# Optimization experiments

Hardware: AMD Instinct MI355X
Metric: run time of the kernel (lower is better)

## Reference

```python
import jax, jax.numpy as jnp
import numpy as np

N_NODES = 50000
N_EDGES = 800000
N_GRAPHS = 256
F_IN = 75  # num_features_xd


def _lin_params(key, fan_in, fan_out):
    kw, kb = jax.random.split(key)
    s = 1.0 / np.sqrt(fan_in)
    W = jax.random.uniform(kw, (fan_in, fan_out), jnp.float32, -s, s)
    b = jax.random.uniform(kb, (fan_out,), jnp.float32, -s, s)
    return W, b


def setup_inputs() -> dict:
    key = jax.random.key(0)
    ks = jax.random.split(key, 8)
    x = jax.random.normal(ks[0], (N_NODES, F_IN), jnp.float32)
    edge_index = jax.random.randint(ks[1], (2, N_EDGES), 0, N_NODES, jnp.int32)
    batch = jnp.sort(jax.random.randint(ks[2], (N_NODES,), 0, N_GRAPHS, jnp.int32))
    W1, b1 = _lin_params(ks[3], F_IN, F_IN)            # conv1: 75 -> 75
    W2, b2 = _lin_params(ks[4], F_IN, 2 * F_IN)        # conv2: 75 -> 150
    W3, b3 = _lin_params(ks[5], 2 * F_IN, 4 * F_IN)    # conv3: 150 -> 300
    Wg1, bg1 = _lin_params(ks[6], 4 * F_IN, 1024)      # fc_g1: 300 -> 1024
    Wg2, bg2 = _lin_params(ks[7], 1024, 128)           # fc_g2: 1024 -> 128
    return dict(x=x, edge_index=edge_index, batch=batch,
                W1=W1, b1=b1, W2=W2, b2=b2, W3=W3, b3=b3,
                Wg1=Wg1, bg1=bg1, Wg2=Wg2, bg2=bg2)


def gcn_conv(x, W, b, src, dst, n):
    """PyG GCNConv: out = D^{-1/2}(A+I)D^{-1/2} X W + b (symmetric norm, self loops)."""
    h = x @ W                                   # [n, out]
    loop = jnp.arange(n, dtype=src.dtype)
    s = jnp.concatenate([src, loop])            # [E+n]
    d = jnp.concatenate([dst, loop])
    deg = jax.ops.segment_sum(jnp.ones(s.shape[0], x.dtype), d, num_segments=n)
    dinv = jnp.where(deg > 0, jax.lax.rsqrt(jnp.maximum(deg, 1e-12)), 0.0)
    norm = dinv[s] * dinv[d]                    # [E+n]
    out = jax.ops.segment_sum(norm[:, None] * h[s], d, num_segments=n)
    return out + b


def reference(x, edge_index, batch, W1, b1, W2, b2, W3, b3, Wg1, bg1, Wg2, bg2):
    src, dst = edge_index[0], edge_index[1]
    n = x.shape[0]
    h = jax.nn.relu(gcn_conv(x, W1, b1, src, dst, n))
    h = jax.nn.relu(gcn_conv(h, W2, b2, src, dst, n))
    h = jax.nn.relu(gcn_conv(h, W3, b3, src, dst, n))
    g = jax.ops.segment_max(h, batch, num_segments=N_GRAPHS)  # global max pool
    g = jax.nn.relu(g @ Wg1 + bg1)
    # dropout is identity in eval mode
    return g @ Wg2 + bg2
```

## Files before the change

### kernel.cpp

```cpp
#include <hip/hip_runtime.h>
#include <math.h>

#define SCAN_B 1024

typedef __attribute__((ext_vector_type(8))) short short8v;
typedef __attribute__((ext_vector_type(8))) unsigned short ushort8v;
typedef __attribute__((ext_vector_type(4))) float f32x4;

static inline int ceil_div_i(long long a, int b) { return (int)((a + b - 1) / b); }

__device__ __forceinline__ unsigned short f2bf(float x) {
    unsigned int u = __float_as_uint(x);
    u += 0x7fffu + ((u >> 16) & 1u);
    return (unsigned short)(u >> 16);
}
__device__ __forceinline__ float bf2f(unsigned short h) {
    return __uint_as_float(((unsigned int)h) << 16);
}
__device__ __forceinline__ ushort8v zero8() {
    ushort8v z;
#pragma unroll
    for (int e = 0; e < 8; e++) z[e] = 0;
    return z;
}


__global__ __launch_bounds__(256) void k_count(const int* __restrict__ dst, int E,
                                               int* __restrict__ cnt) {
    int i = blockIdx.x * blockDim.x + threadIdx.x;
    if (i < E) atomicAdd(&cnt[dst[i]], 1);
}

__global__ __launch_bounds__(256) void k_dinv(const int* __restrict__ cnt,
                                              float* __restrict__ dinv, int N) {
    int i = blockIdx.x * blockDim.x + threadIdx.x;
    if (i < N) dinv[i] = (float)(1.0 / sqrt((double)(cnt[i] + 1)));
}

__global__ __launch_bounds__(256) void k_scan1(const int* __restrict__ cnt,
                                               int* __restrict__ rowptr,
                                               int* __restrict__ bsum, int N) {
    __shared__ int s[256];
    int tid = threadIdx.x;
    int base = blockIdx.x * SCAN_B + tid * 4;
    int a0 = (base + 0 < N) ? cnt[base + 0] : 0;
    int a1 = (base + 1 < N) ? cnt[base + 1] : 0;
    int a2 = (base + 2 < N) ? cnt[base + 2] : 0;
    int a3 = (base + 3 < N) ? cnt[base + 3] : 0;
    int tsum = a0 + a1 + a2 + a3;
    s[tid] = tsum;
    __syncthreads();
    for (int off = 1; off < 256; off <<= 1) {
        int val = 0;
        if (tid >= off) val = s[tid - off];
        __syncthreads();
        if (tid >= off) s[tid] += val;
        __syncthreads();
    }
    int texcl = s[tid] - tsum;
    if (tid == 255) bsum[blockIdx.x] = s[255];
    if (base + 0 < N) rowptr[base + 0] = texcl;
    if (base + 1 < N) rowptr[base + 1] = texcl + a0;
    if (base + 2 < N) rowptr[base + 2] = texcl + a0 + a1;
    if (base + 3 < N) rowptr[base + 3] = texcl + a0 + a1 + a2;
}

__global__ __launch_bounds__(256) void k_scan2(int* __restrict__ bsum, int NB) {
    __shared__ int s[256];
    int tid = threadIdx.x;
    int v = (tid < NB) ? bsum[tid] : 0;
    s[tid] = v;
    __syncthreads();
    for (int off = 1; off < 256; off <<= 1) {
        int val = 0;
        if (tid >= off) val = s[tid - off];
        __syncthreads();
        if (tid >= off) s[tid] += val;
        __syncthreads();
    }
    if (tid < NB) bsum[tid] = s[tid] - v;
}

__global__ __launch_bounds__(256) void k_scan3(int* __restrict__ rowptr,
                                               const int* __restrict__ bsum, int N, int E) {
    int i = blockIdx.x * blockDim.x + threadIdx.x;
    if (i < N) rowptr[i] += bsum[i >> 10];
    if (i == 0) rowptr[N] = E;
}

__global__ __launch_bounds__(256) void k_fill(const int* __restrict__ src,
                                              const int* __restrict__ dst, int E,
                                              const int* __restrict__ rowptr,
                                              int* __restrict__ fill,
                                              int* __restrict__ col) {
    int e = blockIdx.x * blockDim.x + threadIdx.x;
    if (e >= E) return;
    int s = src[e], d = dst[e];
    int pos = atomicAdd(&fill[d], 1);
    col[rowptr[d] + pos] = s;
}


__global__ __launch_bounds__(256) void k_xscale(const float* __restrict__ x,
                                                const float* __restrict__ dinv,
                                                unsigned short* __restrict__ xb,
                                                int N, int F, int XS) {
    int i = blockIdx.x * blockDim.x + threadIdx.x;
    int v = i / XS, c = i - v * XS;
    if (v >= N) return;
    float val = (c < F) ? dinv[v] * x[(size_t)v * F + c] : 0.f;
    xb[i] = f2bf(val);
}


template <int CHUNKS, int SLOTS, int UNR>
__global__ __launch_bounds__(256) void k_gather_s(const unsigned short* __restrict__ Xb,
                                                  const int* __restrict__ rowptr,
                                                  const int* __restrict__ col,
                                                  unsigned short* __restrict__ Th,
                                                  unsigned short* __restrict__ Tl,
                                                  int N, int XS, int KPf) {
    const int v = blockIdx.x * 4 + (threadIdx.x >> 6);
    const int lane = threadIdx.x & 63;
    if (v >= N) return;
    constexpr int VW = 8;
    const int slot = lane / CHUNKS;
    const int chunk = lane - slot * CHUNKS;
    const bool act = lane < CHUNKS * SLOTS;
    const int f0 = chunk * VW;

    float acc[VW];
#pragma unroll
    for (int u = 0; u < VW; u++) acc[u] = 0.f;
    if (slot == 0) {
        ushort8v h = *(const ushort8v*)(Xb + (size_t)v * XS + f0);
#pragma unroll
        for (int u = 0; u < VW; u++) acc[u] = bf2f(h[u]);
    }

    const int beg = rowptr[v], end = rowptr[v + 1];
    for (int jb = beg; jb < end; jb += 64) {
        const int nj = min(64, end - jb);
        int ec = 0;
        if (lane < nj) ec = col[jb + lane];
        for (int e = 0; e < nj; e += SLOTS * UNR) {
            int cs[UNR];
            bool vs[UNR];
#pragma unroll
            for (int u = 0; u < UNR; u++) {
                int srcl = e + u * SLOTS + slot;
                vs[u] = act && (srcl < nj);
                cs[u] = __shfl(ec, srcl & 63);
            }
            ushort8v xv[UNR];
#pragma unroll
            for (int u = 0; u < UNR; u++) {
                xv[u] = zero8();
                if (vs[u]) xv[u] = *(const ushort8v*)(Xb + (size_t)cs[u] * XS + f0);
            }
#pragma unroll
            for (int u = 0; u < UNR; u++)
#pragma unroll
                for (int k2 = 0; k2 < VW; k2++)
                    acc[k2] += bf2f(xv[u][k2]);
        }
    }

#pragma unroll
    for (int k2 = 0; k2 < VW; k2++) {
        float t2 = acc[k2];
#pragma unroll
        for (int s2 = 1; s2 < SLOTS; s2++) t2 += __shfl(acc[k2], chunk + s2 * CHUNKS);
        acc[k2] = t2;
    }

    if (slot == 0 && f0 < KPf) {
        ushort8v h8, l8;
#pragma unroll
        for (int u = 0; u < VW; u++) {
            unsigned short hh = f2bf(acc[u]);
            h8[u] = hh;
            l8[u] = f2bf(acc[u] - bf2f(hh));
        }
        *(ushort8v*)(Th + (size_t)v * KPf + f0) = h8;
        *(ushort8v*)(Tl + (size_t)v * KPf + f0) = l8;
    }
}


__global__ __launch_bounds__(256) void k_wsplit(const float* __restrict__ W,
                                                unsigned short* __restrict__ Wth,
                                                unsigned short* __restrict__ Wtl,
                                                int K, int Fout, int KP) {
    int i = blockIdx.x * blockDim.x + threadIdx.x;
    if (i >= Fout * KP) return;
    int c = i / KP, k = i - c * KP;
    float w = (k < K) ? W[(size_t)k * Fout + c] : 0.f;
    unsigned short h = f2bf(w);
    Wth[i] = h;
    Wtl[i] = f2bf(w - bf2f(h));
}


template <int MODE>
__global__ __launch_bounds__(256) void k_gemm_mfma(
    const unsigned short* __restrict__ Ah, const unsigned short* __restrict__ Al, int KPf,
    const unsigned short* __restrict__ Bth, const unsigned short* __restrict__ Btl,
    const float* __restrict__ bias, const float* __restrict__ dinvp,
    unsigned short* __restrict__ Cb, int CSbf,
    const int* __restrict__ batch, float* __restrict__ G,
    int N, int KP, int Fout) {
    __shared__ unsigned short sAh[128 * 32];
    __shared__ unsigned short sAl[128 * 32];
    __shared__ unsigned short sBh[128 * 32];
    __shared__ unsigned short sBl[128 * 32];
    __shared__ int sBatch[128];

    const int t = threadIdx.x;
    const int r0 = blockIdx.x * 128;
    const int c0 = blockIdx.y * 128;
    const int lane = t & 63;
    const int wv = t >> 6;
    const int wrow = (wv >> 1) * 64;
    const int wcol = (wv & 1) * 64;
    const int l15 = lane & 15;
    const int nt = KP >> 5;

    const int srow = t >> 1;
    const int sseg = (t & 1) << 4;
    const int ltile = srow >> 4;
    const int g0 = sseg >> 3;
    const int wo0 = ltile * 512 + ((srow & 15) + 16 * g0) * 8;
    const int wo1 = ltile * 512 + ((srow & 15) + 16 * (g0 + 1)) * 8;

    if (MODE == 1 && t < 128) sBatch[t] = (r0 + t < N) ? batch[r0 + t] : -1;

    const bool arow_ok = (r0 + srow) < N;
    const bool bcol_ok = (c0 + srow) < Fout;
    const unsigned short* ahRow = Ah + (size_t)(r0 + srow) * KPf;
    const unsigned short* alRow = Al + (size_t)(r0 + srow) * KPf;
    const unsigned short* bhRow = Bth + (size_t)(c0 + srow) * KP;
    const unsigned short* blRow = Btl + (size_t)(c0 + srow) * KP;

    ushort8v rah0, rah1, ral0, ral1, rbh0, rbh1, rbl0, rbl1;

    auto gload = [&](int kk) {
        int gk = kk + sseg;
        bool ok0 = arow_ok && (gk < KPf);
        bool ok1 = arow_ok && (gk + 8 < KPf);
        rah0 = ok0 ? *(const ushort8v*)(ahRow + gk) : zero8();
        rah1 = ok1 ? *(const ushort8v*)(ahRow + gk + 8) : zero8();
        ral0 = ok0 ? *(const ushort8v*)(alRow + gk) : zero8();
        ral1 = ok1 ? *(const ushort8v*)(alRow + gk + 8) : zero8();
        if (bcol_ok) {
            rbh0 = *(const ushort8v*)(bhRow + gk);
            rbh1 = *(const ushort8v*)(bhRow + gk + 8);
            rbl0 = *(const ushort8v*)(blRow + gk);
            rbl1 = *(const ushort8v*)(blRow + gk + 8);
        } else {
            rbh0 = zero8(); rbh1 = zero8(); rbl0 = zero8(); rbl1 = zero8();
        }
    };

    auto wlds = [&]() {
        *(ushort8v*)&sAh[wo0] = rah0;
        *(ushort8v*)&sAh[wo1] = rah1;
        *(ushort8v*)&sAl[wo0] = ral0;
        *(ushort8v*)&sAl[wo1] = ral1;
        *(ushort8v*)&sBh[wo0] = rbh0;
        *(ushort8v*)&sBh[wo1] = rbh1;
        *(ushort8v*)&sBl[wo0] = rbl0;
        *(ushort8v*)&sBl[wo1] = rbl1;
    };

    f32x4 acc[4][4];
#pragma unroll
    for (int i = 0; i < 4; i++)
#pragma unroll
        for (int j = 0; j < 4; j++) acc[i][j] = (f32x4){0.f, 0.f, 0.f, 0.f};

    const int atile = wrow >> 4;
    const int btile = wcol >> 4;
    const int lo = lane * 8;

    gload(0);
    for (int tc = 0; tc < nt; ++tc) {
        wlds();
        __syncthreads();
        if (tc + 1 < nt) gload((tc + 1) * 32);
        short8v ah[4], al[4];
#pragma unroll
        for (int i = 0; i < 4; i++) {
            ah[i] = *(const short8v*)&sAh[(atile + i) * 512 + lo];
            al[i] = *(const short8v*)&sAl[(atile + i) * 512 + lo];
        }
#pragma unroll
        for (int j = 0; j < 4; j++) {
            short8v bh = *(const short8v*)&sBh[(btile + j) * 512 + lo];
            short8v bl = *(const short8v*)&sBl[(btile + j) * 512 + lo];
#pragma unroll
            for (int i = 0; i < 4; i++) {
                acc[i][j] = __builtin_amdgcn_mfma_f32_16x16x32_bf16(al[i], bh, acc[i][j], 0, 0, 0);
                acc[i][j] = __builtin_amdgcn_mfma_f32_16x16x32_bf16(ah[i], bl, acc[i][j], 0, 0, 0);
                acc[i][j] = __builtin_amdgcn_mfma_f32_16x16x32_bf16(ah[i], bh, acc[i][j], 0, 0, 0);
            }
        }
        __syncthreads();
    }

    float drw[16];
#pragma unroll
    for (int i = 0; i < 4; i++)
#pragma unroll
        for (int q = 0; q < 4; q++) {
            int gr = r0 + wrow + i * 16 + (lane >> 4) * 4 + q;
            drw[i * 4 + q] = (gr < N) ? dinvp[gr] : 0.f;
        }

    if (MODE == 0) {
#pragma unroll
        for (int j = 0; j < 4; j++) {
            int gc = c0 + wcol + j * 16 + l15;
            if (gc >= CSbf) continue;
            float bv = (gc < Fout) ? bias[gc] : 0.f;
#pragma unroll
            for (int i = 0; i < 4; i++) {
                int rb = r0 + wrow + i * 16 + (lane >> 4) * 4;
#pragma unroll
                for (int q = 0; q < 4; q++) {
                    int gr = rb + q;
                    if (gr >= N) continue;
                    float dr = drw[i * 4 + q];
                    float vv = (gc < Fout) ? fmaxf(fmaf(acc[i][j][q], dr, bv), 0.f) * dr : 0.f;
                    Cb[(size_t)gr * CSbf + gc] = f2bf(vv);
                }
            }
        }
    } else {
#pragma unroll
        for (int j = 0; j < 4; j++) {
            int gc = c0 + wcol + j * 16 + l15;
            if (gc >= Fout) continue;
            float bv = bias[gc];
            int gcur = -1;
            float vmax = 0.f;
#pragma unroll
            for (int i = 0; i < 4; i++) {
                int lr = wrow + i * 16 + (lane >> 4) * 4;
#pragma unroll
                for (int q = 0; q < 4; q++) {
                    int g = sBatch[lr + q];
                    float vv = fmaxf(fmaf(acc[i][j][q], drw[i * 4 + q], bv), 0.f);
                    if (g < 0) continue;
                    if (g != gcur) {
                        if (gcur >= 0)
                            atomicMax((int*)&G[(size_t)gcur * Fout + gc], __float_as_int(vmax));
                        gcur = g;
                        vmax = vv;
                    } else {
                        vmax = fmaxf(vmax, vv);
                    }
                }
            }
            if (gcur >= 0) atomicMax((int*)&G[(size_t)gcur * Fout + gc], __float_as_int(vmax));
        }
    }
}


__global__ __launch_bounds__(256) void k_fc1(const float* __restrict__ A,
                                             const float* __restrict__ W,
                                             const float* __restrict__ bias,
                                             float* __restrict__ C,
                                             int M, int K, int Nout) {
    __shared__ float sA[2 * 304];
    const int t = threadIdx.x;
    const int m0 = blockIdx.x * 2;
    const int oc = blockIdx.y * 256 + t;

    for (int i = t; i < 2 * K; i += 256) {
        int r = i / K, k = i - r * K;
        sA[r * 304 + k] = (m0 + r < M) ? A[(size_t)(m0 + r) * K + k] : 0.f;
    }
    __syncthreads();

    float acc0 = 0.f, acc1 = 0.f;
    int k = 0;
    for (; k + 8 <= K; k += 8) {
        float w[8];
#pragma unroll
        for (int u = 0; u < 8; u++) w[u] = W[(size_t)(k + u) * Nout + oc];
#pragma unroll
        for (int u = 0; u < 8; u++) {
            acc0 = fmaf(sA[k + u], w[u], acc0);
            acc1 = fmaf(sA[304 + k + u], w[u], acc1);
        }
    }
    for (; k < K; k++) {
        float w = W[(size_t)k * Nout + oc];
        acc0 = fmaf(sA[k], w, acc0);
        acc1 = fmaf(sA[304 + k], w, acc1);
    }
    float bv = bias[oc];
    if (m0 < M) C[(size_t)m0 * Nout + oc] = fmaxf(acc0 + bv, 0.f);
    if (m0 + 1 < M) C[(size_t)(m0 + 1) * Nout + oc] = fmaxf(acc1 + bv, 0.f);
}


__global__ __launch_bounds__(256) void k_fc2p(const float* __restrict__ A,
                                              const float* __restrict__ W,
                                              float* __restrict__ P,
                                              int M, int K, int Nout) {
    __shared__ float sA[2 * 256];
    const int t = threadIdx.x;
    const int m0 = blockIdx.x * 2;
    const int sk = blockIdx.y;
    const int k0 = sk * 256;
    const int row = t >> 7;
    const int oc = t & 127;

    for (int i = t; i < 2 * 256; i += 256) {
        int r = i >> 8, k = i & 255;
        sA[i] = (m0 + r < M) ? A[(size_t)(m0 + r) * K + k0 + k] : 0.f;
    }
    __syncthreads();

    const float* a = sA + row * 256;
    float acc = 0.f;
    for (int k = 0; k < 256; k += 8) {
        float w[8];
#pragma unroll
        for (int u = 0; u < 8; u++) w[u] = W[(size_t)(k0 + k + u) * Nout + oc];
#pragma unroll
        for (int u = 0; u < 8; u++) acc = fmaf(a[k + u], w[u], acc);
    }
    int m = m0 + row;
    if (m < M) P[((size_t)sk * M + m) * Nout + oc] = acc;
}

__global__ __launch_bounds__(256) void k_fc2r(const float* __restrict__ P,
                                              const float* __restrict__ bias,
                                              float* __restrict__ C,
                                              int M, int Nout, int SK) {
    int i = blockIdx.x * blockDim.x + threadIdx.x;
    if (i >= M * Nout) return;
    int oc = i % Nout;
    float acc = bias[oc];
    for (int s2 = 0; s2 < SK; s2++) acc += P[(size_t)s2 * M * Nout + i];
    C[i] = acc;
}


extern "C" void kernel_launch(void* const* d_in, const int* in_sizes, int n_in,
                              void* d_out, int out_size, void* d_ws, size_t ws_size,
                              hipStream_t stream) {
    const float* x     = (const float*)d_in[0];
    const int*   ei    = (const int*)d_in[1];
    const int*   batch = (const int*)d_in[2];
    const float* W1 = (const float*)d_in[3];
    const float* b1 = (const float*)d_in[4];
    const float* W2 = (const float*)d_in[5];
    const float* b2 = (const float*)d_in[6];
    const float* W3 = (const float*)d_in[7];
    const float* b3 = (const float*)d_in[8];
    const float* Wg1 = (const float*)d_in[9];
    const float* bg1 = (const float*)d_in[10];
    const float* Wg2 = (const float*)d_in[11];
    const float* bg2 = (const float*)d_in[12];

    const int N  = in_sizes[2];
    const int E  = in_sizes[1] / 2;
    const int F1 = in_sizes[4];
    const int F2 = in_sizes[6];
    const int F3 = in_sizes[8];
    const int H1 = in_sizes[10];
    const int OC = in_sizes[12];
    const int NG = out_size / OC;
    const int FIN = in_sizes[3] / F1;

    const int KP1 = 96,  KPf1 = 80;
    const int KP3 = 160, KPf3 = 152;
    const int XS0 = 80;
    const int HS1 = 80;
    const int HS2 = 152;

    const int* src = ei;
    const int* dst = ei + E;

    char* base = (char*)d_ws;
    size_t off = 0;
    auto alloc = [&](size_t bytes) -> void* {
        void* p = base + off;
        off = (off + bytes + 255) & ~(size_t)255;
        return p;
    };
    int*   cnt    = (int*)alloc((size_t)N * 4);
    int*   fill   = (int*)alloc((size_t)N * 4);
    int*   rowptr = (int*)alloc((size_t)(N + 1) * 4);
    float* dinv   = (float*)alloc((size_t)N * 4);
    int*   bsum   = (int*)alloc(256 * 4);
    int*   col    = (int*)alloc((size_t)E * 4);
    unsigned short* W1th = (unsigned short*)alloc((size_t)F1 * KP1 * 2);
    unsigned short* W1tl = (unsigned short*)alloc((size_t)F1 * KP1 * 2);
    unsigned short* W2th = (unsigned short*)alloc((size_t)F2 * KP1 * 2);
    unsigned short* W2tl = (unsigned short*)alloc((size_t)F2 * KP1 * 2);
    unsigned short* W3th = (unsigned short*)alloc((size_t)F3 * KP3 * 2);
    unsigned short* W3tl = (unsigned short*)alloc((size_t)F3 * KP3 * 2);
    float* Gb  = (float*)alloc((size_t)NG * F3 * 4);
    float* g1  = (float*)alloc((size_t)NG * H1 * 4);
    float* P2  = (float*)alloc((size_t)4 * NG * OC * 4);
    unsigned short* TgH = (unsigned short*)alloc((size_t)N * KPf3 * 2);
    unsigned short* TgL = (unsigned short*)alloc((size_t)N * KPf3 * 2);
    unsigned short* Xb  = (unsigned short*)alloc((size_t)N * XS0 * 2);
    unsigned short* H1b = (unsigned short*)alloc((size_t)N * HS1 * 2);
    unsigned short* H2b = (unsigned short*)alloc((size_t)N * HS2 * 2);

    hipMemsetAsync(cnt, 0, (size_t)N * 4, stream);
    hipMemsetAsync(fill, 0, (size_t)N * 4, stream);
    hipMemsetAsync(Gb, 0, (size_t)NG * F3 * 4, stream);

    k_count<<<ceil_div_i(E, 256), 256, 0, stream>>>(dst, E, cnt);
    k_dinv<<<ceil_div_i(N, 256), 256, 0, stream>>>(cnt, dinv, N);
    int NB = ceil_div_i(N, SCAN_B);
    k_scan1<<<NB, 256, 0, stream>>>(cnt, rowptr, bsum, N);
    k_scan2<<<1, 256, 0, stream>>>(bsum, NB);
    k_scan3<<<ceil_div_i(N, 256), 256, 0, stream>>>(rowptr, bsum, N, E);
    k_fill<<<ceil_div_i(E, 256), 256, 0, stream>>>(src, dst, E, rowptr, fill, col);

    k_wsplit<<<ceil_div_i((long long)F1 * KP1, 256), 256, 0, stream>>>(W1, W1th, W1tl, FIN, F1, KP1);
    k_wsplit<<<ceil_div_i((long long)F2 * KP1, 256), 256, 0, stream>>>(W2, W2th, W2tl, F1, F2, KP1);
    k_wsplit<<<ceil_div_i((long long)F3 * KP3, 256), 256, 0, stream>>>(W3, W3th, W3tl, F2, F3, KP3);
    k_xscale<<<ceil_div_i((long long)N * XS0, 256), 256, 0, stream>>>(x, dinv, Xb, N, FIN, XS0);

    dim3 blk(256);
    int gw = ceil_div_i(N, 4);
    int gx = ceil_div_i(N, 128);

    k_gather_s<10, 6, 2><<<gw, blk, 0, stream>>>(Xb, rowptr, col, TgH, TgL, N, XS0, KPf1);
    {
        dim3 g(gx, ceil_div_i(F1, 128));
        k_gemm_mfma<0><<<g, blk, 0, stream>>>(TgH, TgL, KPf1, W1th, W1tl, b1, dinv, H1b, HS1,
                                              nullptr, nullptr, N, KP1, F1);
    }
    k_gather_s<10, 6, 2><<<gw, blk, 0, stream>>>(H1b, rowptr, col, TgH, TgL, N, HS1, KPf1);
    {
        dim3 g(gx, ceil_div_i(F2, 128));
        k_gemm_mfma<0><<<g, blk, 0, stream>>>(TgH, TgL, KPf1, W2th, W2tl, b2, dinv, H2b, HS2,
                                              nullptr, nullptr, N, KP1, F2);
    }
    k_gather_s<19, 3, 4><<<gw, blk, 0, stream>>>(H2b, rowptr, col, TgH, TgL, N, HS2, KPf3);
    {
        dim3 g(gx, ceil_div_i(F3, 128));
        k_gemm_mfma<1><<<g, blk, 0, stream>>>(TgH, TgL, KPf3, W3th, W3tl, b3, dinv, nullptr, 0,
                                              batch, Gb, N, KP3, F3);
    }

    {
        dim3 g(ceil_div_i(NG, 2), H1 / 256);
        k_fc1<<<g, 256, 0, stream>>>(Gb, Wg1, bg1, g1, NG, F3, H1);
    }
    {
        dim3 g(ceil_div_i(NG, 2), 4);
        k_fc2p<<<g, 256, 0, stream>>>(g1, Wg2, P2, NG, H1, OC);
        k_fc2r<<<ceil_div_i((long long)NG * OC, 256), 256, 0, stream>>>(
            P2, bg2, (float*)d_out, NG, OC, 4);
    }
}
```

Measured before the change: 350.3 us.

## Keep full weight tile resident in LDS and stream A rows from registers

Replaces the tiled double-buffered LDS GEMM with a kernel that loads the whole 128-column weight slice (high and low bf16 parts) into shared memory once. Each wave then reads its own A rows straight from global memory into registers. The K dimension becomes a compile-time template, and activation strides are padded to a multiple of 32 so the boundary checks go away. The gather kernels are retuned to the padded widths. This drops the per-k-step barriers and the A staging through LDS, at the cost of larger LDS use per block, which may lower occupancy, and extra bytes for the padded rows.

```diff
diff --git a/kernel.cpp b/kernel.cpp
--- a/kernel.cpp
+++ b/kernel.cpp
@@ -202,18 +202,17 @@
 }
 
 
-template <int MODE>
-__global__ __launch_bounds__(256) void k_gemm_mfma(
-    const unsigned short* __restrict__ Ah, const unsigned short* __restrict__ Al, int KPf,
+template <int NT, int MODE>
+__global__ __launch_bounds__(256) void k_gemm_br(
+    const unsigned short* __restrict__ Ah, const unsigned short* __restrict__ Al,
     const unsigned short* __restrict__ Bth, const unsigned short* __restrict__ Btl,
     const float* __restrict__ bias, const float* __restrict__ dinvp,
     unsigned short* __restrict__ Cb, int CSbf,
     const int* __restrict__ batch, float* __restrict__ G,
-    int N, int KP, int Fout) {
-    __shared__ unsigned short sAh[128 * 32];
-    __shared__ unsigned short sAl[128 * 32];
-    __shared__ unsigned short sBh[128 * 32];
-    __shared__ unsigned short sBl[128 * 32];
+    int N, int Fout) {
+    constexpr int KP = NT * 32;
+    constexpr int PL = 8 * NT * 512;
+    __shared__ unsigned short sB[2 * PL];
     __shared__ int sBatch[128];
 
     const int t = threadIdx.x;
@@ -221,96 +220,66 @@
     const int c0 = blockIdx.y * 128;
     const int lane = t & 63;
     const int wv = t >> 6;
-    const int wrow = (wv >> 1) * 64;
-    const int wcol = (wv & 1) * 64;
     const int l15 = lane & 15;
-    const int nt = KP >> 5;
-
-    const int srow = t >> 1;
-    const int sseg = (t & 1) << 4;
-    const int ltile = srow >> 4;
-    const int g0 = sseg >> 3;
-    const int wo0 = ltile * 512 + ((srow & 15) + 16 * g0) * 8;
-    const int wo1 = ltile * 512 + ((srow & 15) + 16 * (g0 + 1)) * 8;
-
+    const int lg = lane >> 4;
+
+    constexpr int KG = KP >> 3;
+    for (int i = t; i < 128 * KG; i += 256) {
+        int colc = i / KG, kg = i - colc * KG;
+        int gc = c0 + colc;
+        ushort8v h = zero8(), l = zero8();
+        if (gc < Fout) {
+            h = *(const ushort8v*)(Bth + (size_t)gc * KP + kg * 8);
+            l = *(const ushort8v*)(Btl + (size_t)gc * KP + kg * 8);
+        }
+        int jt = colc >> 4, tc = kg >> 2, g = kg & 3;
+        int off = (jt * NT + tc) * 512 + ((colc & 15) + 16 * g) * 8;
+        *(ushort8v*)&sB[off] = h;
+        *(ushort8v*)&sB[PL + off] = l;
+    }
     if (MODE == 1 && t < 128) sBatch[t] = (r0 + t < N) ? batch[r0 + t] : -1;
-
-    const bool arow_ok = (r0 + srow) < N;
-    const bool bcol_ok = (c0 + srow) < Fout;
-    const unsigned short* ahRow = Ah + (size_t)(r0 + srow) * KPf;
-    const unsigned short* alRow = Al + (size_t)(r0 + srow) * KPf;
-    const unsigned short* bhRow = Bth + (size_t)(c0 + srow) * KP;
-    const unsigned short* blRow = Btl + (size_t)(c0 + srow) * KP;
-
-    ushort8v rah0, rah1, ral0, ral1, rbh0, rbh1, rbl0, rbl1;
-
-    auto gload = [&](int kk) {
-        int gk = kk + sseg;
-        bool ok0 = arow_ok && (gk < KPf);
-        bool ok1 = arow_ok && (gk + 8 < KPf);
-        rah0 = ok0 ? *(const ushort8v*)(ahRow + gk) : zero8();
-        rah1 = ok1 ? *(const ushort8v*)(ahRow + gk + 8) : zero8();
-        ral0 = ok0 ? *(const ushort8v*)(alRow + gk) : zero8();
-        ral1 = ok1 ? *(const ushort8v*)(alRow + gk + 8) : zero8();
-        if (bcol_ok) {
-            rbh0 = *(const ushort8v*)(bhRow + gk);
-            rbh1 = *(const ushort8v*)(bhRow + gk + 8);
-            rbl0 = *(const ushort8v*)(blRow + gk);
-            rbl1 = *(const ushort8v*)(blRow + gk + 8);
-        } else {
-            rbh0 = zero8(); rbh1 = zero8(); rbl0 = zero8(); rbl1 = zero8();
-        }
-    };
-
-    auto wlds = [&]() {
-        *(ushort8v*)&sAh[wo0] = rah0;
-        *(ushort8v*)&sAh[wo1] = rah1;
-        *(ushort8v*)&sAl[wo0] = ral0;
-        *(ushort8v*)&sAl[wo1] = ral1;
-        *(ushort8v*)&sBh[wo0] = rbh0;
-        *(ushort8v*)&sBh[wo1] = rbh1;
-        *(ushort8v*)&sBl[wo0] = rbl0;
-        *(ushort8v*)&sBl[wo1] = rbl1;
-    };
-
-    f32x4 acc[4][4];
-#pragma unroll
-    for (int i = 0; i < 4; i++)
-#pragma unroll
-        for (int j = 0; j < 4; j++) acc[i][j] = (f32x4){0.f, 0.f, 0.f, 0.f};
-
-    const int atile = wrow >> 4;
-    const int btile = wcol >> 4;
-    const int lo = lane * 8;
-
-    gload(0);
-    for (int tc = 0; tc < nt; ++tc) {
-        wlds();
-        __syncthreads();
-        if (tc + 1 < nt) gload((tc + 1) * 32);
-        short8v ah[4], al[4];
-#pragma unroll
-        for (int i = 0; i < 4; i++) {
-            ah[i] = *(const short8v*)&sAh[(atile + i) * 512 + lo];
-            al[i] = *(const short8v*)&sAl[(atile + i) * 512 + lo];
-        }
-#pragma unroll
-        for (int j = 0; j < 4; j++) {
-            short8v bh = *(const short8v*)&sBh[(btile + j) * 512 + lo];
-            short8v bl = *(const short8v*)&sBl[(btile + j) * 512 + lo];
-#pragma unroll
-            for (int i = 0; i < 4; i++) {
-                acc[i][j] = __builtin_amdgcn_mfma_f32_16x16x32_bf16(al[i], bh, acc[i][j], 0, 0, 0);
-                acc[i][j] = __builtin_amdgcn_mfma_f32_16x16x32_bf16(ah[i], bl, acc[i][j], 0, 0, 0);
-                acc[i][j] = __builtin_amdgcn_mfma_f32_16x16x32_bf16(ah[i], bh, acc[i][j], 0, 0, 0);
-            }
-        }
-        __syncthreads();
-    }
-
-    float drw[16];
-#pragma unroll
-    for (int i = 0; i < 4; i++)
+    __syncthreads();
+
+    const int wrow = wv * 32;
+    const int row0 = r0 + wrow + l15;
+    const int row1 = row0 + 16;
+    const bool ok0 = row0 < N;
+    const bool ok1 = row1 < N;
+    const unsigned short* a0h = Ah + (size_t)row0 * KP;
+    const unsigned short* a0l = Al + (size_t)row0 * KP;
+    const unsigned short* a1h = Ah + (size_t)row1 * KP;
+    const unsigned short* a1l = Al + (size_t)row1 * KP;
+
+    f32x4 acc[2][8];
+#pragma unroll
+    for (int i = 0; i < 2; i++)
+#pragma unroll
+        for (int j = 0; j < 8; j++) acc[i][j] = (f32x4){0.f, 0.f, 0.f, 0.f};
+
+#pragma unroll 2
+    for (int tc = 0; tc < NT; ++tc) {
+        const int ko = tc * 32 + lg * 8;
+        short8v A0h = ok0 ? *(const short8v*)(a0h + ko) : (short8v)zero8();
+        short8v A0l = ok0 ? *(const short8v*)(a0l + ko) : (short8v)zero8();
+        short8v A1h = ok1 ? *(const short8v*)(a1h + ko) : (short8v)zero8();
+        short8v A1l = ok1 ? *(const short8v*)(a1l + ko) : (short8v)zero8();
+#pragma unroll
+        for (int j = 0; j < 8; j++) {
+            const int off = (j * NT + tc) * 512 + lane * 8;
+            short8v bh = *(const short8v*)&sB[off];
+            short8v bl = *(const short8v*)&sB[PL + off];
+            acc[0][j] = __builtin_amdgcn_mfma_f32_16x16x32_bf16(A0l, bh, acc[0][j], 0, 0, 0);
+            acc[0][j] = __builtin_amdgcn_mfma_f32_16x16x32_bf16(A0h, bl, acc[0][j], 0, 0, 0);
+            acc[0][j] = __builtin_amdgcn_mfma_f32_16x16x32_bf16(A0h, bh, acc[0][j], 0, 0, 0);
+            acc[1][j] = __builtin_amdgcn_mfma_f32_16x16x32_bf16(A1l, bh, acc[1][j], 0, 0, 0);
+            acc[1][j] = __builtin_amdgcn_mfma_f32_16x16x32_bf16(A1h, bl, acc[1][j], 0, 0, 0);
+            acc[1][j] = __builtin_amdgcn_mfma_f32_16x16x32_bf16(A1h, bh, acc[1][j], 0, 0, 0);
+        }
+    }
+
+    float drw[8];
+#pragma unroll
+    for (int i = 0; i < 2; i++)
 #pragma unroll
         for (int q = 0; q < 4; q++) {
             int gr = r0 + wrow + i * 16 + (lane >> 4) * 4 + q;
@@ -319,12 +288,12 @@
 
     if (MODE == 0) {
 #pragma unroll
-        for (int j = 0; j < 4; j++) {
-            int gc = c0 + wcol + j * 16 + l15;
+        for (int j = 0; j < 8; j++) {
+            int gc = c0 + j * 16 + l15;
             if (gc >= CSbf) continue;
             float bv = (gc < Fout) ? bias[gc] : 0.f;
 #pragma unroll
-            for (int i = 0; i < 4; i++) {
+            for (int i = 0; i < 2; i++) {
                 int rb = r0 + wrow + i * 16 + (lane >> 4) * 4;
 #pragma unroll
                 for (int q = 0; q < 4; q++) {
@@ -338,14 +307,14 @@
         }
     } else {
 #pragma unroll
-        for (int j = 0; j < 4; j++) {
-            int gc = c0 + wcol + j * 16 + l15;
+        for (int j = 0; j < 8; j++) {
+            int gc = c0 + j * 16 + l15;
             if (gc >= Fout) continue;
             float bv = bias[gc];
             int gcur = -1;
             float vmax = 0.f;
 #pragma unroll
-            for (int i = 0; i < 4; i++) {
+            for (int i = 0; i < 2; i++) {
                 int lr = wrow + i * 16 + (lane >> 4) * 4;
 #pragma unroll
                 for (int q = 0; q < 4; q++) {
@@ -478,11 +447,8 @@
     const int NG = out_size / OC;
     const int FIN = in_sizes[3] / F1;
 
-    const int KP1 = 96,  KPf1 = 80;
-    const int KP3 = 160, KPf3 = 152;
-    const int XS0 = 80;
-    const int HS1 = 80;
-    const int HS2 = 152;
+    const int KP1 = 96;
+    const int KP3 = 160;
 
     const int* src = ei;
     const int* dst = ei + E;
@@ -509,11 +475,11 @@
     float* Gb  = (float*)alloc((size_t)NG * F3 * 4);
     float* g1  = (float*)alloc((size_t)NG * H1 * 4);
     float* P2  = (float*)alloc((size_t)4 * NG * OC * 4);
-    unsigned short* TgH = (unsigned short*)alloc((size_t)N * KPf3 * 2);
-    unsigned short* TgL = (unsigned short*)alloc((size_t)N * KPf3 * 2);
-    unsigned short* Xb  = (unsigned short*)alloc((size_t)N * XS0 * 2);
-    unsigned short* H1b = (unsigned short*)alloc((size_t)N * HS1 * 2);
-    unsigned short* H2b = (unsigned short*)alloc((size_t)N * HS2 * 2);
+    unsigned short* TgH = (unsigned short*)alloc((size_t)N * KP3 * 2);
+    unsigned short* TgL = (unsigned short*)alloc((size_t)N * KP3 * 2);
+    unsigned short* Xb  = (unsigned short*)alloc((size_t)N * KP1 * 2);
+    unsigned short* H1b = (unsigned short*)alloc((size_t)N * KP1 * 2);
+    unsigned short* H2b = (unsigned short*)alloc((size_t)N * KP3 * 2);
 
     hipMemsetAsync(cnt, 0, (size_t)N * 4, stream);
     hipMemsetAsync(fill, 0, (size_t)N * 4, stream);
@@ -530,29 +496,29 @@
     k_wsplit<<<ceil_div_i((long long)F1 * KP1, 256), 256, 0, stream>>>(W1, W1th, W1tl, FIN, F1, KP1);
     k_wsplit<<<ceil_div_i((long long)F2 * KP1, 256), 256, 0, stream>>>(W2, W2th, W2tl, F1, F2, KP1);
     k_wsplit<<<ceil_div_i((long long)F3 * KP3, 256), 256, 0, stream>>>(W3, W3th, W3tl, F2, F3, KP3);
-    k_xscale<<<ceil_div_i((long long)N * XS0, 256), 256, 0, stream>>>(x, dinv, Xb, N, FIN, XS0);
+    k_xscale<<<ceil_div_i((long long)N * KP1, 256), 256, 0, stream>>>(x, dinv, Xb, N, FIN, KP1);
 
     dim3 blk(256);
     int gw = ceil_div_i(N, 4);
     int gx = ceil_div_i(N, 128);
 
-    k_gather_s<10, 6, 2><<<gw, blk, 0, stream>>>(Xb, rowptr, col, TgH, TgL, N, XS0, KPf1);
+    k_gather_s<12, 5, 2><<<gw, blk, 0, stream>>>(Xb, rowptr, col, TgH, TgL, N, KP1, KP1);
     {
         dim3 g(gx, ceil_div_i(F1, 128));
-        k_gemm_mfma<0><<<g, blk, 0, stream>>>(TgH, TgL, KPf1, W1th, W1tl, b1, dinv, H1b, HS1,
-                                              nullptr, nullptr, N, KP1, F1);
-    }
-    k_gather_s<10, 6, 2><<<gw, blk, 0, stream>>>(H1b, rowptr, col, TgH, TgL, N, HS1, KPf1);
+        k_gemm_br<3, 0><<<g, blk, 0, stream>>>(TgH, TgL, W1th, W1tl, b1, dinv, H1b, KP1,
+                                               nullptr, nullptr, N, F1);
+    }
+    k_gather_s<12, 5, 2><<<gw, blk, 0, stream>>>(H1b, rowptr, col, TgH, TgL, N, KP1, KP1);
     {
         dim3 g(gx, ceil_div_i(F2, 128));
-        k_gemm_mfma<0><<<g, blk, 0, stream>>>(TgH, TgL, KPf1, W2th, W2tl, b2, dinv, H2b, HS2,
-                                              nullptr, nullptr, N, KP1, F2);
-    }
-    k_gather_s<19, 3, 4><<<gw, blk, 0, stream>>>(H2b, rowptr, col, TgH, TgL, N, HS2, KPf3);
+        k_gemm_br<3, 0><<<g, blk, 0, stream>>>(TgH, TgL, W2th, W2tl, b2, dinv, H2b, KP3,
+                                               nullptr, nullptr, N, F2);
+    }
+    k_gather_s<20, 3, 4><<<gw, blk, 0, stream>>>(H2b, rowptr, col, TgH, TgL, N, KP3, KP3);
     {
         dim3 g(gx, ceil_div_i(F3, 128));
-        k_gemm_mfma<1><<<g, blk, 0, stream>>>(TgH, TgL, KPf3, W3th, W3tl, b3, dinv, nullptr, 0,
-                                              batch, Gb, N, KP3, F3);
+        k_gemm_br<5, 1><<<g, blk, 0, stream>>>(TgH, TgL, W3th, W3tl, b3, dinv, nullptr, 0,
+                                               batch, Gb, N, F3);
     }
 
     {
```

Measured after the change: 379.2 us. 8.3% more time.
